# Optimization experiments

Measured on AMD Instinct MI355X. Metric: run time of the kernel, lower is better.

The kernel has to match this reference:

```python
import jax, jax.numpy as jnp
import numpy as np

B, T, C = 2, 2048, 1024
H = 16
D = C // H  # 64
SCALE = 1.0 / np.sqrt(D)


def setup_inputs() -> dict:
    key = jax.random.key(0)
    k1, k2, k3 = jax.random.split(key, 3)
    x = jax.random.normal(k1, (B, T, C), dtype=jnp.float32)
    Wqkv = jax.random.normal(k2, (C, 3 * C), dtype=jnp.float32) * 0.02
    bqkv = jnp.zeros((3 * C,), dtype=jnp.float32)
    Wo = jax.random.normal(k3, (C, C), dtype=jnp.float32) * 0.02
    bo = jnp.zeros((C,), dtype=jnp.float32)
    return {"x": x, "Wqkv": Wqkv, "bqkv": bqkv, "Wo": Wo, "bo": bo}


def reference(x, Wqkv, bqkv, Wo, bo):
    Bsz, Tlen, Cdim = x.shape
    qkv = x @ Wqkv + bqkv                       # [B,T,3C]
    qkv = qkv.reshape(Bsz, Tlen, 3, H, D)
    qkv = jnp.transpose(qkv, (2, 0, 3, 1, 4))   # [3,B,H,T,D]
    q, k, v = qkv[0], qkv[1], qkv[2]
    att = jnp.einsum("bhqd,bhkd->bhqk", q, k) * SCALE
    # NOTE: faithful to source: mask keeps positions where k >= q
    i = jnp.arange(Tlen)
    mask = i[None, :] >= i[:, None]             # [T,T], entry [q,k]: k >= q
    att = jnp.where(mask[None, None], att, -jnp.inf)
    att = jax.nn.softmax(att, axis=-1)
    # dropout p=0.0 (inference) -> identity
    y = jnp.einsum("bhqk,bhkd->bhqd", att, v)   # [B,H,T,D]
    y = jnp.transpose(y, (0, 2, 1, 3)).reshape(Bsz, Tlen, Cdim)
    y = y @ Wo + bo
    return y
```

## Files before the change

kernel.cpp:

```cpp
#include <hip/hip_runtime.h>
#include <hip/hip_bf16.h>
#include <cstdint>
#include <cstddef>

typedef __bf16 bf16_t;
typedef __bf16 bf16x8 __attribute__((ext_vector_type(8)));
typedef __bf16 bf16x4 __attribute__((ext_vector_type(4)));
typedef short short4v __attribute__((ext_vector_type(4)));
typedef float f32x4 __attribute__((ext_vector_type(4)));

#define NB 2
#define NT 2048
#define NC 1024
#define NH 16
#define ND 64
#define NM (NB * NT)
#define N3 (3 * NC)
#define QSCALE_LOG2E 0.18033688011112042f

#define GLOAD_LDS16(gptr, lptr)                                                          \
  __builtin_amdgcn_global_load_lds((const __attribute__((address_space(1))) void*)(gptr), \
                                   (__attribute__((address_space(3))) void*)(lptr), 16, 0, 0)

__global__ __launch_bounds__(256) void cast_f32_bf16_k(const float* __restrict__ in,
                                                       bf16_t* __restrict__ out, int n) {
  int i = (blockIdx.x * 256 + threadIdx.x) * 4;
  if (i + 3 < n) {
    const float4 v = *(const float4*)(in + i);
    bf16x4 o;
    o[0] = (bf16_t)v.x; o[1] = (bf16_t)v.y; o[2] = (bf16_t)v.z; o[3] = (bf16_t)v.w;
    *(bf16x4*)(out + i) = o;
  }
}

__global__ __launch_bounds__(256) void transpose_cast_k(const float* __restrict__ in,
                                                        bf16_t* __restrict__ out,
                                                        int R, int Ccols) {
  __shared__ float tile[32][33];
  int tc = blockIdx.x * 32;
  int tr = blockIdx.y * 32;
  int lx = threadIdx.x & 31;
  int ly = threadIdx.x >> 5;
#pragma unroll
  for (int i = 0; i < 32; i += 8)
    tile[ly + i][lx] = in[(size_t)(tr + ly + i) * Ccols + tc + lx];
  __syncthreads();
#pragma unroll
  for (int i = 0; i < 32; i += 8)
    out[(size_t)(tc + ly + i) * R + tr + lx] = (bf16_t)tile[lx][ly + i];
}

template <int K>
__device__ __forceinline__ void gemm_mainloop(const bf16_t* __restrict__ A,
                                              const bf16_t* __restrict__ Bt,
                                              int m0, int n0, f32x4 acc[4][4],
                                              bf16_t* lds) {
  bf16_t* As = lds;
  bf16_t* Bs = lds + 4096;
  const int tid = threadIdx.x;
  const int lane = tid & 63;
  const int w = tid >> 6;
  const int wm = (w & 1) * 64;
  const int wn = (w >> 1) * 64;
  const int quad = lane >> 4;
  const int l16 = lane & 15;

  for (int k0 = 0; k0 < K; k0 += 32) {
#pragma unroll
    for (int i = 0; i < 2; ++i) {
      const int gb = w * 128 + i * 64;
      const int g = gb + lane;
      GLOAD_LDS16(A + (size_t)(m0 + (g >> 2)) * K + k0 + (g & 3) * 8, As + gb * 8);
      GLOAD_LDS16(Bt + (size_t)(n0 + (g >> 2)) * K + k0 + (g & 3) * 8, Bs + gb * 8);
    }
    __syncthreads();
    bf16x8 af[4], bfr[4];
#pragma unroll
    for (int i = 0; i < 4; ++i)
      af[i] = *(const bf16x8*)(As + (wm + i * 16 + l16) * 32 + quad * 8);
#pragma unroll
    for (int j = 0; j < 4; ++j)
      bfr[j] = *(const bf16x8*)(Bs + (wn + j * 16 + l16) * 32 + quad * 8);
#pragma unroll
    for (int i = 0; i < 4; ++i)
#pragma unroll
      for (int j = 0; j < 4; ++j)
        acc[i][j] = __builtin_amdgcn_mfma_f32_16x16x32_bf16(af[i], bfr[j], acc[i][j], 0, 0, 0);
    __syncthreads();
  }
}

__global__ __launch_bounds__(256) void qkv_gemm_k(const bf16_t* __restrict__ A,
                                                  const bf16_t* __restrict__ Bt,
                                                  const float* __restrict__ bias,
                                                  bf16_t* __restrict__ qb,
                                                  bf16_t* __restrict__ kb,
                                                  bf16_t* __restrict__ vb) {
  __shared__ __align__(16) bf16_t lds[8192];
  const int m0 = blockIdx.y * 128, n0 = blockIdx.x * 128;
  f32x4 acc[4][4] = {};
  gemm_mainloop<NC>(A, Bt, m0, n0, acc, lds);

  const int lane = threadIdx.x & 63;
  const int w = threadIdx.x >> 6;
  const int wm = (w & 1) * 64, wn = (w >> 1) * 64;
  const int quad = lane >> 4, l16 = lane & 15;
#pragma unroll
  for (int i = 0; i < 4; ++i)
#pragma unroll
    for (int j = 0; j < 4; ++j) {
      const int n = n0 + wn + j * 16 + l16;
      const float bn = bias[n];
      const int which = n >> 10;
      const int rem = n & 1023;
      const int h = rem >> 6, d = rem & 63;
      bf16_t* dst = (which == 0) ? qb : (which == 1) ? kb : vb;
      const float sc = (which == 0) ? QSCALE_LOG2E : 1.0f;
#pragma unroll
      for (int r = 0; r < 4; ++r) {
        const int m = m0 + wm + i * 16 + quad * 4 + r;
        const int b = m >> 11, t = m & 2047;
        const size_t bh = (size_t)b * NH + h;
        dst[(bh * NT + t) * ND + d] = (bf16_t)((acc[i][j][r] + bn) * sc);
      }
    }
}

__global__ __launch_bounds__(256) void vtile_k(const bf16_t* __restrict__ v,
                                               bf16_t* __restrict__ vt2) {
  const int bh = blockIdx.x >> 5, c = blockIdx.x & 31;
  const bf16_t* src = v + ((size_t)bh * NT + c * 64) * ND;
  bf16_t* dst = vt2 + ((size_t)bh * 32 + c) * 4096;
#pragma unroll
  for (int it = 0; it < 4; ++it) {
    const int slot = it * 256 + threadIdx.x;
    const int g = slot >> 6, d = slot & 63;
    bf16x4 val;
#pragma unroll
    for (int j = 0; j < 4; ++j) val[j] = src[(size_t)(g * 4 + j) * ND + d];
    *(bf16x4*)(dst + (size_t)slot * 4) = val;
  }
}

__global__ __launch_bounds__(256, 4) void attn_k(const bf16_t* __restrict__ q,
                                                 const bf16_t* __restrict__ k,
                                                 const bf16_t* __restrict__ vt2,
                                                 bf16_t* __restrict__ y ) {
  const int bh = blockIdx.x & 31;
  const int u = (blockIdx.x >> 5) & 7;
  const int r4 = blockIdx.x >> 8;
  const int T = r4 * 8 + ((r4 & 1) ? (7 - u) : u);
  const int b = bh >> 4, h = bh & 15;

  const bf16_t* qp = q + (size_t)bh * NT * ND;
  const bf16_t* kp = k + (size_t)bh * NT * ND;
  const bf16_t* vp = vt2 + (size_t)bh * 32 * 4096;

  __shared__ __align__(16) bf16_t kbuf[2][4096];
  __shared__ __align__(16) bf16_t vbuf[2][4096];

  const int lane = threadIdx.x & 63;
  const int w = threadIdx.x >> 6;
  const int quad = lane >> 4, l16 = lane & 15;
  const int qv = T * 64 + w * 16 + l16;

  const bf16x8 qf0 = *(const bf16x8*)(qp + (size_t)qv * ND + quad * 8);
  const bf16x8 qf1 = *(const bf16x8*)(qp + (size_t)qv * ND + 32 + quad * 8);

  float m = -INFINITY, l = 0.f;
  f32x4 o[4];
#pragma unroll
  for (int dj = 0; dj < 4; ++dj) o[dj] = (f32x4){0.f, 0.f, 0.f, 0.f};

  auto stage = [&](int c, int bi) {
    const bf16_t* kc = kp + (size_t)c * 64 * ND;
    const bf16_t* vc = vp + (size_t)c * 4096;
#pragma unroll
    for (int i = 0; i < 2; ++i) {
      const int gb = w * 128 + i * 64;
      const int s = gb + lane;
      const int row = s >> 3;
      const int cs = (s & 7) ^ (row & 7);
      GLOAD_LDS16(kc + ((size_t)row * 8 + cs) * 8, kbuf[bi] + gb * 8);
      GLOAD_LDS16(vc + (size_t)s * 8, vbuf[bi] + gb * 8);
    }
  };

  stage(T, 0);
  int cur = 0;
  for (int c = T; c < 32; ++c) {
    __syncthreads();
    if (c + 1 < 32) stage(c + 1, cur ^ 1);

    const bf16_t* kt = kbuf[cur];
    const bf16_t* vt = vbuf[cur];
    const int t0 = c * 64;

    f32x4 sv[4];
#pragma unroll
    for (int kj = 0; kj < 4; ++kj) {
      const int kr = kj * 16 + l16;
      const int sw = kr & 7;
      const bf16x8 a0 = *(const bf16x8*)(kt + ((size_t)kr * 8 + (quad ^ sw)) * 8);
      const bf16x8 a1 = *(const bf16x8*)(kt + ((size_t)kr * 8 + ((4 + quad) ^ sw)) * 8);
      f32x4 z = {0.f, 0.f, 0.f, 0.f};
      z = __builtin_amdgcn_mfma_f32_16x16x32_bf16(a0, qf0, z, 0, 0, 0);
      z = __builtin_amdgcn_mfma_f32_16x16x32_bf16(a1, qf1, z, 0, 0, 0);
      sv[kj] = z;
    }
    if (c == T) {
#pragma unroll
      for (int kj = 0; kj < 4; ++kj)
#pragma unroll
        for (int r = 0; r < 4; ++r)
          if (t0 + kj * 16 + quad * 4 + r < qv) sv[kj][r] = -INFINITY;
    }
    float mx = -INFINITY;
#pragma unroll
    for (int kj = 0; kj < 4; ++kj)
#pragma unroll
      for (int r = 0; r < 4; ++r) mx = fmaxf(mx, sv[kj][r]);
    mx = fmaxf(mx, __shfl_xor(mx, 16));
    mx = fmaxf(mx, __shfl_xor(mx, 32));
    const float mnew = fmaxf(m, mx);
    const float alpha = exp2f(m - mnew);
    m = mnew;
    float rs = 0.f;
#pragma unroll
    for (int kj = 0; kj < 4; ++kj)
#pragma unroll
      for (int r = 0; r < 4; ++r) {
        const float p = exp2f(sv[kj][r] - mnew);
        sv[kj][r] = p;
        rs += p;
      }
    rs += __shfl_xor(rs, 16);
    rs += __shfl_xor(rs, 32);
    l = l * alpha + rs;
    short4v pf[4];
#pragma unroll
    for (int kj = 0; kj < 4; ++kj) {
      bf16x4 pb;
#pragma unroll
      for (int r = 0; r < 4; ++r) pb[r] = (bf16_t)sv[kj][r];
      pf[kj] = __builtin_bit_cast(short4v, pb);
    }
#pragma unroll
    for (int dj = 0; dj < 4; ++dj) {
      o[dj][0] *= alpha; o[dj][1] *= alpha; o[dj][2] *= alpha; o[dj][3] *= alpha;
#pragma unroll
      for (int kj = 0; kj < 4; ++kj) {
        const bf16x4 a =
            *(const bf16x4*)(vt + ((size_t)(kj * 4 + quad) * 64 + dj * 16 + l16) * 4);
        o[dj] = __builtin_amdgcn_mfma_f32_16x16x16bf16_1k(
            __builtin_bit_cast(short4v, a), pf[kj], o[dj], 0, 0, 0);
      }
    }
    cur ^= 1;
  }

  const float inv = 1.0f / l;
  const size_t base = ((size_t)b * NT + qv) * NC + h * 64;
#pragma unroll
  for (int dj = 0; dj < 4; ++dj) {
    bf16x4 va;
#pragma unroll
    for (int r = 0; r < 4; ++r) va[r] = (bf16_t)(o[dj][r] * inv);
    *(bf16x4*)(y + base + dj * 16 + quad * 4) = va;
  }
}

__global__ __launch_bounds__(256) void out_gemm_k(const bf16_t* __restrict__ A,
                                                  const bf16_t* __restrict__ Bt,
                                                  const float* __restrict__ bias,
                                                  float* __restrict__ out) {
  __shared__ __align__(16) bf16_t lds[8192];
  const int m0 = blockIdx.y * 128, n0 = blockIdx.x * 128;
  f32x4 acc[4][4] = {};
  gemm_mainloop<NC>(A, Bt, m0, n0, acc, lds);

  const int lane = threadIdx.x & 63;
  const int w = threadIdx.x >> 6;
  const int wm = (w & 1) * 64, wn = (w >> 1) * 64;
  const int quad = lane >> 4, l16 = lane & 15;
#pragma unroll
  for (int i = 0; i < 4; ++i)
#pragma unroll
    for (int j = 0; j < 4; ++j) {
      const int n = n0 + wn + j * 16 + l16;
      const float bn = bias[n];
#pragma unroll
      for (int r = 0; r < 4; ++r) {
        const int m = m0 + wm + i * 16 + quad * 4 + r;
        out[(size_t)m * NC + n] = acc[i][j][r] + bn;
      }
    }
}

extern "C" void kernel_launch(void* const* d_in, const int* in_sizes, int n_in,
                              void* d_out, int out_size, void* d_ws, size_t ws_size,
                              hipStream_t stream) {
  const float* x = (const float*)d_in[0];
  const float* Wqkv = (const float*)d_in[1];
  const float* bqkv = (const float*)d_in[2];
  const float* Wo = (const float*)d_in[3];
  const float* bo = (const float*)d_in[4];
  float* out = (float*)d_out;

  char* p = (char*)d_ws;
  bf16_t* xbf = (bf16_t*)p;   p += (size_t)NM * NC * sizeof(bf16_t);
  bf16_t* wqkvT = (bf16_t*)p; p += (size_t)N3 * NC * sizeof(bf16_t);
  bf16_t* woT = (bf16_t*)p;   p += (size_t)NC * NC * sizeof(bf16_t);
  bf16_t* qb = (bf16_t*)p;    p += (size_t)NB * NH * NT * ND * sizeof(bf16_t);
  bf16_t* kb = (bf16_t*)p;    p += (size_t)NB * NH * NT * ND * sizeof(bf16_t);
  bf16_t* vb = (bf16_t*)p;    p += (size_t)NB * NH * NT * ND * sizeof(bf16_t);
  bf16_t* yb = (bf16_t*)p;    p += (size_t)NM * NC * sizeof(bf16_t);
  bf16_t* vt2 = xbf;

  hipLaunchKernelGGL(cast_f32_bf16_k, dim3(NM * NC / 1024), dim3(256), 0, stream,
                     x, xbf, NM * NC);
  hipLaunchKernelGGL(transpose_cast_k, dim3(N3 / 32, NC / 32), dim3(256), 0, stream,
                     Wqkv, wqkvT, NC, N3);
  hipLaunchKernelGGL(transpose_cast_k, dim3(NC / 32, NC / 32), dim3(256), 0, stream,
                     Wo, woT, NC, NC);
  hipLaunchKernelGGL(qkv_gemm_k, dim3(N3 / 128, NM / 128), dim3(256), 0, stream,
                     xbf, wqkvT, bqkv, qb, kb, vb);
  hipLaunchKernelGGL(vtile_k, dim3(32 * 32), dim3(256), 0, stream, vb, vt2);
  hipLaunchKernelGGL(attn_k, dim3(1024), dim3(256), 0, stream, qb, kb, vt2, yb);
  hipLaunchKernelGGL(out_gemm_k, dim3(NC / 128, NM / 128), dim3(256), 0, stream,
                     yb, woT, bo, out);
}
```

Baseline: 194.6 us.

## Fuse V tiling into QKV epilogue, merge weight transposes, pair query tiles in attention

The QKV GEMM epilogue now writes V straight into the tiled transposed layout, which removes the separate vtile kernel. The two weight transpose launches are merged into one kernel. Each attention block now processes two adjacent 64-row query tiles that share the same K/V loads from LDS, so there are half as many blocks and launch bounds drop to 2 blocks per SM. The softmax row sum is now computed with an MFMA against a vector of ones, and the alpha rescale is skipped when no lane's max changed. These trade fewer launches and less K/V traffic for higher register pressure and lower occupancy.

```diff
diff --git a/kernel.cpp b/kernel.cpp
--- a/kernel.cpp
+++ b/kernel.cpp
@@ -33,21 +33,27 @@
   }
 }
 
-__global__ __launch_bounds__(256) void transpose_cast_k(const float* __restrict__ in,
-                                                        bf16_t* __restrict__ out,
-                                                        int R, int Ccols) {
+__global__ __launch_bounds__(256) void transposeW_k(const float* __restrict__ Wqkv,
+                                                    const float* __restrict__ Wo,
+                                                    bf16_t* __restrict__ wqkvT,
+                                                    bf16_t* __restrict__ woT) {
   __shared__ float tile[32][33];
-  int tc = blockIdx.x * 32;
-  int tr = blockIdx.y * 32;
-  int lx = threadIdx.x & 31;
-  int ly = threadIdx.x >> 5;
+  const int bx = blockIdx.x;
+  const float* in;
+  bf16_t* out;
+  int Ccols, tc;
+  if (bx < 96) { in = Wqkv; out = wqkvT; Ccols = 3072; tc = bx * 32; }
+  else         { in = Wo;   out = woT;   Ccols = 1024; tc = (bx - 96) * 32; }
+  const int tr = blockIdx.y * 32;
+  const int lx = threadIdx.x & 31;
+  const int ly = threadIdx.x >> 5;
 #pragma unroll
   for (int i = 0; i < 32; i += 8)
     tile[ly + i][lx] = in[(size_t)(tr + ly + i) * Ccols + tc + lx];
   __syncthreads();
 #pragma unroll
   for (int i = 0; i < 32; i += 8)
-    out[(size_t)(tc + ly + i) * R + tr + lx] = (bf16_t)tile[lx][ly + i];
+    out[(size_t)(tc + ly + i) * 1024 + tr + lx] = (bf16_t)tile[lx][ly + i];
 }
 
 template <int K>
@@ -95,7 +101,7 @@
                                                   const float* __restrict__ bias,
                                                   bf16_t* __restrict__ qb,
                                                   bf16_t* __restrict__ kb,
-                                                  bf16_t* __restrict__ vb) {
+                                                  bf16_t* __restrict__ vt2) {
   __shared__ __align__(16) bf16_t lds[8192];
   const int m0 = blockIdx.y * 128, n0 = blockIdx.x * 128;
   f32x4 acc[4][4] = {};
@@ -114,42 +120,34 @@
       const int which = n >> 10;
       const int rem = n & 1023;
       const int h = rem >> 6, d = rem & 63;
-      bf16_t* dst = (which == 0) ? qb : (which == 1) ? kb : vb;
-      const float sc = (which == 0) ? QSCALE_LOG2E : 1.0f;
-#pragma unroll
-      for (int r = 0; r < 4; ++r) {
-        const int m = m0 + wm + i * 16 + quad * 4 + r;
-        const int b = m >> 11, t = m & 2047;
-        const size_t bh = (size_t)b * NH + h;
-        dst[(bh * NT + t) * ND + d] = (bf16_t)((acc[i][j][r] + bn) * sc);
-      }
-    }
-}
-
-__global__ __launch_bounds__(256) void vtile_k(const bf16_t* __restrict__ v,
-                                               bf16_t* __restrict__ vt2) {
-  const int bh = blockIdx.x >> 5, c = blockIdx.x & 31;
-  const bf16_t* src = v + ((size_t)bh * NT + c * 64) * ND;
-  bf16_t* dst = vt2 + ((size_t)bh * 32 + c) * 4096;
-#pragma unroll
-  for (int it = 0; it < 4; ++it) {
-    const int slot = it * 256 + threadIdx.x;
-    const int g = slot >> 6, d = slot & 63;
-    bf16x4 val;
-#pragma unroll
-    for (int j = 0; j < 4; ++j) val[j] = src[(size_t)(g * 4 + j) * ND + d];
-    *(bf16x4*)(dst + (size_t)slot * 4) = val;
-  }
-}
-
-__global__ __launch_bounds__(256, 4) void attn_k(const bf16_t* __restrict__ q,
+      const int mb = m0 + wm + i * 16 + quad * 4;
+      const int b = mb >> 11, t4 = mb & 2047;
+      const size_t bh = (size_t)b * NH + h;
+      if (which == 2) {
+        const int c = t4 >> 6, g = (t4 >> 2) & 15;
+        bf16x4 val;
+#pragma unroll
+        for (int r = 0; r < 4; ++r) val[r] = (bf16_t)(acc[i][j][r] + bn);
+        *(bf16x4*)(vt2 + ((bh * 32 + c) * 1024 + (size_t)g * 64 + d) * 4) = val;
+      } else {
+        bf16_t* dst = (which == 0) ? qb : kb;
+        const float sc = (which == 0) ? QSCALE_LOG2E : 1.0f;
+#pragma unroll
+        for (int r = 0; r < 4; ++r)
+          dst[(bh * NT + t4 + r) * ND + d] = (bf16_t)((acc[i][j][r] + bn) * sc);
+      }
+    }
+}
+
+__global__ __launch_bounds__(256, 2) void attn_k(const bf16_t* __restrict__ q,
                                                  const bf16_t* __restrict__ k,
                                                  const bf16_t* __restrict__ vt2,
                                                  bf16_t* __restrict__ y ) {
   const int bh = blockIdx.x & 31;
   const int u = (blockIdx.x >> 5) & 7;
-  const int r4 = blockIdx.x >> 8;
-  const int T = r4 * 8 + ((r4 & 1) ? (7 - u) : u);
+  const int r2 = blockIdx.x >> 8;
+  const int a = r2 ? (15 - u) : u;
+  const int cA = 2 * a;
   const int b = bh >> 4, h = bh & 15;
 
   const bf16_t* qp = q + (size_t)bh * NT * ND;
@@ -162,111 +160,152 @@
   const int lane = threadIdx.x & 63;
   const int w = threadIdx.x >> 6;
   const int quad = lane >> 4, l16 = lane & 15;
-  const int qv = T * 64 + w * 16 + l16;
-
-  const bf16x8 qf0 = *(const bf16x8*)(qp + (size_t)qv * ND + quad * 8);
-  const bf16x8 qf1 = *(const bf16x8*)(qp + (size_t)qv * ND + 32 + quad * 8);
-
-  float m = -INFINITY, l = 0.f;
-  f32x4 o[4];
-#pragma unroll
-  for (int dj = 0; dj < 4; ++dj) o[dj] = (f32x4){0.f, 0.f, 0.f, 0.f};
-
-  auto stage = [&](int c, int bi) {
-    const bf16_t* kc = kp + (size_t)c * 64 * ND;
-    const bf16_t* vc = vp + (size_t)c * 4096;
+  const int qvA = cA * 64 + w * 16 + l16;
+  const int qvB = qvA + 64;
+  const int sw = l16 & 7;
+
+  const bf16x8 qfA0 = *(const bf16x8*)(qp + (size_t)qvA * ND + quad * 8);
+  const bf16x8 qfA1 = *(const bf16x8*)(qp + (size_t)qvA * ND + 32 + quad * 8);
+  const bf16x8 qfB0 = *(const bf16x8*)(qp + (size_t)qvB * ND + quad * 8);
+  const bf16x8 qfB1 = *(const bf16x8*)(qp + (size_t)qvB * ND + 32 + quad * 8);
+
+  const short4v ones = {0x3F80, 0x3F80, 0x3F80, 0x3F80};
+
+  float mA = -INFINITY, lA = 0.f, mB = -INFINITY, lB = 0.f;
+  f32x4 oA[4], oB[4];
+#pragma unroll
+  for (int dj = 0; dj < 4; ++dj) {
+    oA[dj] = (f32x4){0.f, 0.f, 0.f, 0.f};
+    oB[dj] = (f32x4){0.f, 0.f, 0.f, 0.f};
+  }
+
+  auto stage = [&](const bf16_t* kc, const bf16_t* vc, int bi) {
 #pragma unroll
     for (int i = 0; i < 2; ++i) {
       const int gb = w * 128 + i * 64;
       const int s = gb + lane;
       const int row = s >> 3;
       const int cs = (s & 7) ^ (row & 7);
-      GLOAD_LDS16(kc + ((size_t)row * 8 + cs) * 8, kbuf[bi] + gb * 8);
+      GLOAD_LDS16(kc + (size_t)row * 64 + cs * 8, kbuf[bi] + gb * 8);
       GLOAD_LDS16(vc + (size_t)s * 8, vbuf[bi] + gb * 8);
     }
   };
 
-  stage(T, 0);
-  int cur = 0;
-  for (int c = T; c < 32; ++c) {
-    __syncthreads();
-    if (c + 1 < 32) stage(c + 1, cur ^ 1);
-
-    const bf16_t* kt = kbuf[cur];
-    const bf16_t* vt = vbuf[cur];
-    const int t0 = c * 64;
-
-    f32x4 sv[4];
-#pragma unroll
-    for (int kj = 0; kj < 4; ++kj) {
-      const int kr = kj * 16 + l16;
-      const int sw = kr & 7;
-      const bf16x8 a0 = *(const bf16x8*)(kt + ((size_t)kr * 8 + (quad ^ sw)) * 8);
-      const bf16x8 a1 = *(const bf16x8*)(kt + ((size_t)kr * 8 + ((4 + quad) ^ sw)) * 8);
-      f32x4 z = {0.f, 0.f, 0.f, 0.f};
-      z = __builtin_amdgcn_mfma_f32_16x16x32_bf16(a0, qf0, z, 0, 0, 0);
-      z = __builtin_amdgcn_mfma_f32_16x16x32_bf16(a1, qf1, z, 0, 0, 0);
-      sv[kj] = z;
-    }
-    if (c == T) {
-#pragma unroll
-      for (int kj = 0; kj < 4; ++kj)
-#pragma unroll
-        for (int r = 0; r < 4; ++r)
-          if (t0 + kj * 16 + quad * 4 + r < qv) sv[kj][r] = -INFINITY;
-    }
-    float mx = -INFINITY;
-#pragma unroll
-    for (int kj = 0; kj < 4; ++kj)
-#pragma unroll
-      for (int r = 0; r < 4; ++r) mx = fmaxf(mx, sv[kj][r]);
+  auto softmax = [&](f32x4 sv[4], float& m, float& l, short4v pf[4]) -> float {
+    float mx = fmaxf(fmaxf(sv[0][0], sv[0][1]), fmaxf(sv[0][2], sv[0][3]));
+#pragma unroll
+    for (int kj = 1; kj < 4; ++kj)
+      mx = fmaxf(mx, fmaxf(fmaxf(sv[kj][0], sv[kj][1]), fmaxf(sv[kj][2], sv[kj][3])));
     mx = fmaxf(mx, __shfl_xor(mx, 16));
     mx = fmaxf(mx, __shfl_xor(mx, 32));
     const float mnew = fmaxf(m, mx);
     const float alpha = exp2f(m - mnew);
     m = mnew;
-    float rs = 0.f;
-#pragma unroll
-    for (int kj = 0; kj < 4; ++kj)
-#pragma unroll
-      for (int r = 0; r < 4; ++r) {
-        const float p = exp2f(sv[kj][r] - mnew);
-        sv[kj][r] = p;
-        rs += p;
-      }
-    rs += __shfl_xor(rs, 16);
-    rs += __shfl_xor(rs, 32);
-    l = l * alpha + rs;
-    short4v pf[4];
 #pragma unroll
     for (int kj = 0; kj < 4; ++kj) {
       bf16x4 pb;
 #pragma unroll
-      for (int r = 0; r < 4; ++r) pb[r] = (bf16_t)sv[kj][r];
+      for (int r = 0; r < 4; ++r) pb[r] = (bf16_t)exp2f(sv[kj][r] - mnew);
       pf[kj] = __builtin_bit_cast(short4v, pb);
     }
+    f32x4 z = {0.f, 0.f, 0.f, 0.f};
+#pragma unroll
+    for (int kj = 0; kj < 4; ++kj)
+      z = __builtin_amdgcn_mfma_f32_16x16x16bf16_1k(ones, pf[kj], z, 0, 0, 0);
+    if (__any(alpha != 1.0f)) l = l * alpha + z[0]; else l += z[0];
+    return alpha;
+  };
+
+  const bf16_t* kc = kp + (size_t)cA * 4096;
+  const bf16_t* vc = vp + (size_t)cA * 4096;
+  stage(kc, vc, 0);
+  int cur = 0;
+
+  for (int c = cA; c < 32; ++c) {
+    __syncthreads();
+    if (c + 1 < 32) stage(kc + 4096, vc + 4096, cur ^ 1);
+
+    const bf16_t* kt = kbuf[cur];
+    const bf16_t* vt = vbuf[cur];
+    const bool bact = (c > cA);
+    const int t0 = c * 64;
+
+    f32x4 svA[4], svB[4];
+#pragma unroll
+    for (int kj = 0; kj < 4; ++kj) {
+      const int kr = kj * 16 + l16;
+      const bf16x8 a0 = *(const bf16x8*)(kt + ((size_t)kr * 8 + (quad ^ sw)) * 8);
+      const bf16x8 a1 = *(const bf16x8*)(kt + ((size_t)kr * 8 + ((4 + quad) ^ sw)) * 8);
+      f32x4 z = {0.f, 0.f, 0.f, 0.f};
+      z = __builtin_amdgcn_mfma_f32_16x16x32_bf16(a0, qfA0, z, 0, 0, 0);
+      svA[kj] = __builtin_amdgcn_mfma_f32_16x16x32_bf16(a1, qfA1, z, 0, 0, 0);
+      if (bact) {
+        f32x4 zb = {0.f, 0.f, 0.f, 0.f};
+        zb = __builtin_amdgcn_mfma_f32_16x16x32_bf16(a0, qfB0, zb, 0, 0, 0);
+        svB[kj] = __builtin_amdgcn_mfma_f32_16x16x32_bf16(a1, qfB1, zb, 0, 0, 0);
+      }
+    }
+    if (c == cA) {
+#pragma unroll
+      for (int kj = 0; kj < 4; ++kj)
+#pragma unroll
+        for (int r = 0; r < 4; ++r)
+          if (t0 + kj * 16 + quad * 4 + r < qvA) svA[kj][r] = -INFINITY;
+    }
+    if (bact && c == cA + 1) {
+#pragma unroll
+      for (int kj = 0; kj < 4; ++kj)
+#pragma unroll
+        for (int r = 0; r < 4; ++r)
+          if (t0 + kj * 16 + quad * 4 + r < qvB) svB[kj][r] = -INFINITY;
+    }
+
+    short4v pfA[4], pfB[4];
+    const float aA = softmax(svA, mA, lA, pfA);
+    float aB = 1.0f;
+    if (bact) aB = softmax(svB, mB, lB, pfB);
+
+    if (__any(aA != 1.0f)) {
+#pragma unroll
+      for (int dj = 0; dj < 4; ++dj) {
+        oA[dj][0] *= aA; oA[dj][1] *= aA; oA[dj][2] *= aA; oA[dj][3] *= aA;
+      }
+    }
+    if (bact && __any(aB != 1.0f)) {
+#pragma unroll
+      for (int dj = 0; dj < 4; ++dj) {
+        oB[dj][0] *= aB; oB[dj][1] *= aB; oB[dj][2] *= aB; oB[dj][3] *= aB;
+      }
+    }
+
 #pragma unroll
     for (int dj = 0; dj < 4; ++dj) {
-      o[dj][0] *= alpha; o[dj][1] *= alpha; o[dj][2] *= alpha; o[dj][3] *= alpha;
 #pragma unroll
       for (int kj = 0; kj < 4; ++kj) {
-        const bf16x4 a =
+        const bf16x4 vf =
             *(const bf16x4*)(vt + ((size_t)(kj * 4 + quad) * 64 + dj * 16 + l16) * 4);
-        o[dj] = __builtin_amdgcn_mfma_f32_16x16x16bf16_1k(
-            __builtin_bit_cast(short4v, a), pf[kj], o[dj], 0, 0, 0);
-      }
-    }
-    cur ^= 1;
-  }
-
-  const float inv = 1.0f / l;
-  const size_t base = ((size_t)b * NT + qv) * NC + h * 64;
+        const short4v vfs = __builtin_bit_cast(short4v, vf);
+        oA[dj] = __builtin_amdgcn_mfma_f32_16x16x16bf16_1k(vfs, pfA[kj], oA[dj], 0, 0, 0);
+        if (bact)
+          oB[dj] = __builtin_amdgcn_mfma_f32_16x16x16bf16_1k(vfs, pfB[kj], oB[dj], 0, 0, 0);
+      }
+    }
+    kc += 4096; vc += 4096; cur ^= 1;
+  }
+
+  const float invA = 1.0f / lA, invB = 1.0f / lB;
+  const size_t baseA = ((size_t)b * NT + qvA) * NC + h * 64;
+  const size_t baseB = ((size_t)b * NT + qvB) * NC + h * 64;
 #pragma unroll
   for (int dj = 0; dj < 4; ++dj) {
-    bf16x4 va;
-#pragma unroll
-    for (int r = 0; r < 4; ++r) va[r] = (bf16_t)(o[dj][r] * inv);
-    *(bf16x4*)(y + base + dj * 16 + quad * 4) = va;
+    bf16x4 va, vb;
+#pragma unroll
+    for (int r = 0; r < 4; ++r) {
+      va[r] = (bf16_t)(oA[dj][r] * invA);
+      vb[r] = (bf16_t)(oB[dj][r] * invB);
+    }
+    *(bf16x4*)(y + baseA + dj * 16 + quad * 4) = va;
+    *(bf16x4*)(y + baseB + dj * 16 + quad * 4) = vb;
   }
 }
 
@@ -313,20 +352,16 @@
   bf16_t* woT = (bf16_t*)p;   p += (size_t)NC * NC * sizeof(bf16_t);
   bf16_t* qb = (bf16_t*)p;    p += (size_t)NB * NH * NT * ND * sizeof(bf16_t);
   bf16_t* kb = (bf16_t*)p;    p += (size_t)NB * NH * NT * ND * sizeof(bf16_t);
-  bf16_t* vb = (bf16_t*)p;    p += (size_t)NB * NH * NT * ND * sizeof(bf16_t);
+  bf16_t* vt2 = (bf16_t*)p;   p += (size_t)NB * NH * NT * ND * sizeof(bf16_t);
   bf16_t* yb = (bf16_t*)p;    p += (size_t)NM * NC * sizeof(bf16_t);
-  bf16_t* vt2 = xbf;
 
   hipLaunchKernelGGL(cast_f32_bf16_k, dim3(NM * NC / 1024), dim3(256), 0, stream,
                      x, xbf, NM * NC);
-  hipLaunchKernelGGL(transpose_cast_k, dim3(N3 / 32, NC / 32), dim3(256), 0, stream,
-                     Wqkv, wqkvT, NC, N3);
-  hipLaunchKernelGGL(transpose_cast_k, dim3(NC / 32, NC / 32), dim3(256), 0, stream,
-                     Wo, woT, NC, NC);
+  hipLaunchKernelGGL(transposeW_k, dim3(128, 32), dim3(256), 0, stream,
+                     Wqkv, Wo, wqkvT, woT);
   hipLaunchKernelGGL(qkv_gemm_k, dim3(N3 / 128, NM / 128), dim3(256), 0, stream,
-                     xbf, wqkvT, bqkv, qb, kb, vb);
-  hipLaunchKernelGGL(vtile_k, dim3(32 * 32), dim3(256), 0, stream, vb, vt2);
-  hipLaunchKernelGGL(attn_k, dim3(1024), dim3(256), 0, stream, qb, kb, vt2, yb);
+                     xbf, wqkvT, bqkv, qb, kb, vt2);
+  hipLaunchKernelGGL(attn_k, dim3(512), dim3(256), 0, stream, qb, kb, vt2, yb);
   hipLaunchKernelGGL(out_gemm_k, dim3(NC / 128, NM / 128), dim3(256), 0, stream,
                      yb, woT, bo, out);
 }
```

Measured after the change: 238.6 us. 1.23x slower.
